# Optimization experiments

Hardware: AMD Instinct MI355X
Metric: run time of the kernel (lower is better)

## Reference

```python
import jax, jax.numpy as jnp
import numpy as np

B, T, D = 8, 1024, 1024
H = 16
DH = D // H  # 64


def setup_inputs() -> dict:
    key = jax.random.key(0)
    k1, k2, k3 = jax.random.split(key, 3)
    x = jax.random.normal(k1, (B, T, D), dtype=jnp.float32)
    W_qkv = jax.random.normal(k2, (3 * D, D), dtype=jnp.float32) * (D ** -0.5)
    W_proj = jax.random.normal(k3, (D, D), dtype=jnp.float32) * (D ** -0.5)
    return {"x": x, "W_qkv": W_qkv, "W_proj": W_proj}


def reference(x, W_qkv, W_proj):
    b, t, _ = x.shape
    # qkv: [B,T,3*D] -> [B,T,3,H,DH]
    qkv = (x @ W_qkv.T).reshape(b, t, 3, H, DH)
    q, k, v = qkv[:, :, 0], qkv[:, :, 1], qkv[:, :, 2]  # [B,T,H,DH]
    scale = DH ** -0.5
    # scores: [B,H,Tq,Tk]
    scores = jnp.einsum("bqhd,bkhd->bhqk", q, k) * scale
    # NOTE: softmax over dim=-2 (the QUERY axis), as in the original module
    attn = jax.nn.softmax(scores, axis=-2)
    out = jnp.einsum("bhqk,bkhd->bqhd", attn, v).reshape(b, t, D)
    return out @ W_proj.T
```

## Files before the change

### kernel.cpp

```cpp
#include <hip/hip_runtime.h>


typedef __bf16 bf16_t;
typedef __bf16 bf16x8 __attribute__((ext_vector_type(8)));
typedef __bf16 bf16x4 __attribute__((ext_vector_type(4)));
typedef float f32x4 __attribute__((ext_vector_type(4)));
typedef unsigned short u16x8 __attribute__((ext_vector_type(8)));

#define DEV __device__ __forceinline__
#define C2 0.18033688f

DEV void gld_lds16(const bf16_t* g, bf16_t* l) {
  __builtin_amdgcn_global_load_lds(
      (const __attribute__((address_space(1))) unsigned int*)g,
      (__attribute__((address_space(3))) unsigned int*)l, 16, 0, 0);
}

DEV float exp2c(float x) { return __builtin_amdgcn_exp2f(fminf(x, 30.f)); }
DEV float sanit(float v) { return (v == v) ? fminf(fmaxf(v, -1e4f), 1e4f) : 0.f; }

DEV int sw64(int r, int kc) { return r * 64 + (((kc ^ (r + (r >> 3))) & 7) << 3); }

DEV f32x4 mfma16(bf16x8 a, bf16x8 b, f32x4 c) {
  return __builtin_amdgcn_mfma_f32_16x16x32_bf16(a, b, c, 0, 0, 0);
}

__global__ void convert_in(const void* __restrict__ x, const void* __restrict__ wq,
                           const void* __restrict__ wp, bf16_t* __restrict__ xb,
                           bf16_t* __restrict__ wqb, bf16_t* __restrict__ wpb,
                           int* __restrict__ flagp) {
  __shared__ int smax;
  if (threadIdx.x == 0) smax = 0;
  __syncthreads();
  {
    int e = (((const unsigned short*)x)[threadIdx.x] >> 7) & 0xFF;
    atomicMax(&smax, e);
  }
  __syncthreads();
  const bool isF32 = smax >= 160;

  int i = blockIdx.x * 256 + threadIdx.x;
  if (i == 0) *flagp = isF32 ? 1 : 0;
  const void* src;
  bf16_t* dst;
  int off;
  bool isQ = false;
  if (i < 1048576) { src = x; dst = xb; off = i; }
  else if (i < 1441792) {
    src = wq; dst = wqb; off = i - 1048576;
    isQ = off < 131072;
  } else { src = wp; dst = wpb; off = i - 1441792; }
  if (isF32) {
    const float s = isQ ? C2 : 1.0f;
    const float4* sp = (const float4*)src;
    float4 a = sp[off * 2], b = sp[off * 2 + 1];
    bf16x8 o;
    o[0] = (bf16_t)(a.x * s); o[1] = (bf16_t)(a.y * s);
    o[2] = (bf16_t)(a.z * s); o[3] = (bf16_t)(a.w * s);
    o[4] = (bf16_t)(b.x * s); o[5] = (bf16_t)(b.y * s);
    o[6] = (bf16_t)(b.z * s); o[7] = (bf16_t)(b.w * s);
    *(bf16x8*)(dst + (size_t)off * 8) = o;
  } else {
    u16x8 v = ((const u16x8*)src)[off];
    if (isQ) {
      bf16x8 bsrc = __builtin_bit_cast(bf16x8, v);
      bf16x8 o;
#pragma unroll
      for (int t = 0; t < 8; ++t) o[t] = (bf16_t)((float)bsrc[t] * C2);
      *(bf16x8*)(dst + (size_t)off * 8) = o;
    } else {
      ((u16x8*)dst)[off] = v;
    }
  }
}

__global__ __launch_bounds__(256, 2)
void gemm_bt(const bf16_t* __restrict__ A, int lda, const bf16_t* __restrict__ B,
             bf16_t* __restrict__ Cb, float* __restrict__ Cf, int ldc,
             int K, const int* __restrict__ f32flag) {
  __shared__ bf16_t sA0[128 * 64];
  __shared__ bf16_t sB0[128 * 64];
  __shared__ bf16_t sA1[128 * 64];
  __shared__ bf16_t sB1[128 * 64];
  const int tid = threadIdx.x;
  const int wave = tid >> 6, lane = tid & 63;
  const int l = lane & 15, quad = lane >> 4;
  const int nwg = gridDim.x * gridDim.y;
  const int bid = blockIdx.y * gridDim.x + blockIdx.x;
  const int sb = (bid & 7) * (nwg >> 3) + (bid >> 3);
  const int row0 = (sb / gridDim.x) * 128, col0 = (sb % gridDim.x) * 128;
  const int wm = (wave >> 1) * 64, wn = (wave & 1) * 64;
  f32x4 acc[4][4];
#pragma unroll
  for (int i = 0; i < 4; ++i)
#pragma unroll
    for (int j = 0; j < 4; ++j) acc[i][j] = f32x4{0.f, 0.f, 0.f, 0.f};

#define STAGE_G(sa, sb_, kk)                                                  \
  {                                                                           \
    _Pragma("unroll") for (int t = 0; t < 4; ++t) {                           \
      int n = t * 256 + tid;                                                  \
      int r = n >> 3;                                                         \
      int kc = ((n & 7) ^ (r + (r >> 3))) & 7;                                \
      gld_lds16(A + (size_t)(row0 + r) * lda + (kk) + kc * 8, (sa) + n * 8);  \
      gld_lds16(B + (size_t)(col0 + r) * K + (kk) + kc * 8, (sb_) + n * 8);   \
    }                                                                         \
  }

#define COMPUTE_G(sa, sb_)                                                    \
  {                                                                           \
    _Pragma("unroll") for (int ks = 0; ks < 2; ++ks) {                        \
      bf16x8 af[4], bfr[4];                                                   \
      _Pragma("unroll") for (int i = 0; i < 4; ++i) af[i] =                   \
          *(const bf16x8*)&(sa)[sw64(wm + i * 16 + l, ks * 4 + quad)];        \
      _Pragma("unroll") for (int j = 0; j < 4; ++j) bfr[j] =                  \
          *(const bf16x8*)&(sb_)[sw64(wn + j * 16 + l, ks * 4 + quad)];       \
      _Pragma("unroll") for (int i = 0; i < 4; ++i)                           \
          _Pragma("unroll") for (int j = 0; j < 4; ++j) acc[i][j] =           \
              mfma16(af[i], bfr[j], acc[i][j]);                               \
    }                                                                         \
  }

  STAGE_G(sA0, sB0, 0);
  for (int k0 = 0; k0 < K; k0 += 128) {
    __syncthreads();
    if (k0 + 64 < K) STAGE_G(sA1, sB1, k0 + 64);
    COMPUTE_G(sA0, sB0);
    __syncthreads();
    if (k0 + 128 < K) STAGE_G(sA0, sB0, k0 + 128);
    COMPUTE_G(sA1, sB1);
  }
#undef STAGE_G
#undef COMPUTE_G

  const bool of32 = (f32flag != nullptr) && (*f32flag != 0);
#pragma unroll
  for (int i = 0; i < 4; ++i) {
    int rr = row0 + wm + i * 16 + quad * 4;
#pragma unroll
    for (int j = 0; j < 4; ++j) {
      int cc = col0 + wn + j * 16 + l;
#pragma unroll
      for (int t = 0; t < 4; ++t) {
        float v = sanit(acc[i][j][t]);
        size_t idx = (size_t)(rr + t) * ldc + cc;
        if (of32) Cf[idx] = v; else Cb[idx] = (bf16_t)v;
      }
    }
  }
}

__global__ __launch_bounds__(256, 4)
void attn_stats(const bf16_t* __restrict__ qkv, bf16_t* __restrict__ Vts) {
  __shared__ bf16_t sK[128 * 64];
  __shared__ bf16_t sV[128 * 64];
  __shared__ float sL[128];
  const int bh = blockIdx.x, kt = blockIdx.y;
  const int b = bh >> 4, h = bh & 15;
  const int tid = threadIdx.x, wave = tid >> 6, lane = tid & 63;
  const int l = lane & 15, quad = lane >> 4;
  const size_t rowK = (size_t)b * 1024 + kt * 128;

#pragma unroll
  for (int t = 0; t < 4; ++t) {
    int base = wave * 256 + t * 64;
    int n = base + lane;
    int r = n >> 3;
    int kc = ((n & 7) ^ (r + (r >> 3))) & 7;
    gld_lds16(qkv + (rowK + r) * 3072 + 2048 + h * 64 + kc * 8, sV + base * 8);
    gld_lds16(qkv + (rowK + r) * 3072 + 1024 + h * 64 + kc * 8, sK + base * 8);
  }
  if (tid < 128) sL[tid] = 0.f;
  __syncthreads();

  float accj[8];
#pragma unroll
  for (int j = 0; j < 8; ++j) accj[j] = 0.f;

  for (int qt = 0; qt < 8; ++qt) {
    bf16x8 aq[2][2];
#pragma unroll
    for (int i = 0; i < 2; ++i)
#pragma unroll
      for (int ks = 0; ks < 2; ++ks)
        aq[i][ks] = *(const bf16x8*)&qkv[((size_t)b * 1024 + qt * 128 + wave * 32 +
                                          i * 16 + l) * 3072 + h * 64 +
                                         (ks * 4 + quad) * 8];
#pragma unroll
    for (int j = 0; j < 8; ++j) {
      f32x4 s0 = {0.f, 0.f, 0.f, 0.f}, s1 = {0.f, 0.f, 0.f, 0.f};
      __builtin_amdgcn_s_setprio(1);
#pragma unroll
      for (int ks = 0; ks < 2; ++ks) {
        bf16x8 bk = *(const bf16x8*)&sK[sw64(j * 16 + l, ks * 4 + quad)];
        s0 = mfma16(aq[0][ks], bk, s0);
        s1 = mfma16(aq[1][ks], bk, s1);
      }
      __builtin_amdgcn_s_setprio(0);
#pragma unroll
      for (int t = 0; t < 4; ++t)
        accj[j] += exp2c(s0[t]) + exp2c(s1[t]);
    }
  }
#pragma unroll
  for (int j = 0; j < 8; ++j) {
    float v = accj[j];
    v += __shfl_xor(v, 16);
    v += __shfl_xor(v, 32);
    if (lane < 16) atomicAdd(&sL[j * 16 + l], v);
  }
  __syncthreads();
  if (tid < 128) sL[tid] = 1.0f / fmaxf(sL[tid], 1e-20f);
  __syncthreads();

#pragma unroll
  for (int t = 0; t < 4; ++t) {
    int u = t * 256 + tid;
    int d = u >> 4, k0 = (u & 15) * 8;
    bf16x8 pk;
#pragma unroll
    for (int i = 0; i < 8; ++i) {
      int kl = (k0 & ~31) | ((i >> 2) << 4) | (((k0 >> 3) & 3) << 2) | (i & 3);
      float v = (float)sV[sw64(kl, d >> 3) + (d & 7)];
      pk[i] = (bf16_t)(v * sL[kl]);
    }
    *(bf16x8*)&Vts[((size_t)bh * 64 + d) * 1024 + kt * 128 + k0] = pk;
  }
}

__global__ __launch_bounds__(512, 4)
void attn_out_k(const bf16_t* __restrict__ qkv, const bf16_t* __restrict__ Vts,
                bf16_t* __restrict__ attn) {
  __shared__ bf16_t sK[2][128 * 64];
  __shared__ bf16_t sV[2][64 * 128];
  const int bh = blockIdx.x, qt = blockIdx.y;
  const int b = bh >> 4, h = bh & 15;
  const int tid = threadIdx.x, wave = tid >> 6, lane = tid & 63;
  const int l = lane & 15, quad = lane >> 4;
  const bf16_t* qbase = qkv + (size_t)b * 3145728 + h * 64;
  const bf16_t* vbase = Vts + (size_t)bh * 65536;

  bf16x8 bq[2][2];
#pragma unroll
  for (int i = 0; i < 2; ++i)
#pragma unroll
    for (int ks = 0; ks < 2; ++ks)
      bq[i][ks] = *(const bf16x8*)&qbase[(size_t)(qt * 256 + wave * 32 + i * 16 + l) *
                                             3072 + ks * 32 + quad * 8];
  f32x4 o[2][4];
#pragma unroll
  for (int i = 0; i < 2; ++i)
#pragma unroll
    for (int jd = 0; jd < 4; ++jd) o[i][jd] = f32x4{0.f, 0.f, 0.f, 0.f};

#pragma unroll
  for (int t = 0; t < 2; ++t) {
    int n = t * 512 + tid;
    int r = n >> 3;
    int kc = ((n & 7) ^ (r + (r >> 3))) & 7;
    gld_lds16(qkv + ((size_t)b * 1024 + r) * 3072 + 1024 + h * 64 + kc * 8,
              sK[0] + n * 8);
    int d = n >> 4, s = n & 15;
    int c = s ^ (d & 7);
    gld_lds16(vbase + (size_t)d * 1024 + c * 8, sV[0] + n * 8);
  }

  for (int kt = 0; kt < 8; ++kt) {
    const int buf = kt & 1;
    __syncthreads();
    if (kt < 7) {
#pragma unroll
      for (int t = 0; t < 2; ++t) {
        int n = t * 512 + tid;
        int r = n >> 3;
        int kc = ((n & 7) ^ (r + (r >> 3))) & 7;
        gld_lds16(qkv + ((size_t)b * 1024 + (kt + 1) * 128 + r) * 3072 + 1024 +
                      h * 64 + kc * 8,
                  sK[buf ^ 1] + n * 8);
        int d = n >> 4, s = n & 15;
        int c = s ^ (d & 7);
        gld_lds16(vbase + (size_t)d * 1024 + (kt + 1) * 128 + c * 8,
                  sV[buf ^ 1] + n * 8);
      }
    }
    const bf16_t* sKb = sK[buf];
    const bf16_t* sVb = sV[buf];

#pragma unroll
    for (int ch = 0; ch < 4; ++ch) {
      bf16x8 ak[2][2];
#pragma unroll
      for (int kk = 0; kk < 2; ++kk)
#pragma unroll
        for (int ks = 0; ks < 2; ++ks)
          ak[kk][ks] = *(const bf16x8*)&sKb[sw64(ch * 32 + kk * 16 + l,
                                                 ks * 4 + quad)];
      bf16x8 va[4];
#pragma unroll
      for (int jd = 0; jd < 4; ++jd)
        va[jd] = *(const bf16x8*)&sVb[(jd * 16 + l) * 128 +
                                      (((ch * 4 + quad) ^ (l & 7)) << 3)];
#pragma unroll
      for (int i = 0; i < 2; ++i) {
        __builtin_amdgcn_s_setprio(1);
        f32x4 st0 = {0.f, 0.f, 0.f, 0.f}, st1 = {0.f, 0.f, 0.f, 0.f};
        st0 = mfma16(ak[0][0], bq[i][0], st0);
        st0 = mfma16(ak[0][1], bq[i][1], st0);
        st1 = mfma16(ak[1][0], bq[i][0], st1);
        st1 = mfma16(ak[1][1], bq[i][1], st1);
        bf16x8 pc;
#pragma unroll
        for (int t = 0; t < 4; ++t) {
          pc[t] = (bf16_t)exp2c(st0[t]);
          pc[4 + t] = (bf16_t)exp2c(st1[t]);
        }
#pragma unroll
        for (int jd = 0; jd < 4; ++jd)
          o[i][jd] = mfma16(va[jd], pc, o[i][jd]);
        __builtin_amdgcn_s_setprio(0);
      }
    }
  }
#pragma unroll
  for (int i = 0; i < 2; ++i) {
    size_t row = (size_t)b * 1024 + qt * 256 + wave * 32 + i * 16 + l;
#pragma unroll
    for (int jd = 0; jd < 4; ++jd) {
      bf16x4 pk;
#pragma unroll
      for (int t = 0; t < 4; ++t) pk[t] = (bf16_t)sanit(o[i][jd][t]);
      *(bf16x4*)&attn[row * 3072 + h * 64 + jd * 16 + quad * 4] = pk;
    }
  }
}

extern "C" void kernel_launch(void* const* d_in, const int* in_sizes, int n_in,
                              void* d_out, int out_size, void* d_ws, size_t ws_size,
                              hipStream_t stream) {
  (void)in_sizes; (void)n_in; (void)out_size; (void)ws_size;
  char* w = (char*)d_ws;
  bf16_t* qkv = (bf16_t*)w;
  bf16_t* xb = (bf16_t*)(w + 50331648);
  bf16_t* Vts = xb;
  bf16_t* Wqkvb = (bf16_t*)(w + 67108864);
  bf16_t* Wprojb = (bf16_t*)(w + 73400320);
  int* flag = (int*)(w + 75497472);
  bf16_t* attn = qkv + 2048;

  convert_in<<<6144, 256, 0, stream>>>(d_in[0], d_in[1], d_in[2],
                                       xb, Wqkvb, Wprojb, flag);

  gemm_bt<<<dim3(24, 64), 256, 0, stream>>>(xb, 1024, Wqkvb, qkv, nullptr, 3072,
                                            1024, nullptr);
  attn_stats<<<dim3(128, 8), 256, 0, stream>>>(qkv, Vts);
  attn_out_k<<<dim3(128, 4), 512, 0, stream>>>(qkv, Vts, attn);
  gemm_bt<<<dim3(8, 64), 256, 0, stream>>>(attn, 3072, Wprojb, (bf16_t*)d_out,
                                           (float*)d_out, 1024, 1024, flag);
}
```

Measured before the change: 262.9 us.

## Double-buffer Q tiles through LDS in attention stats kernel

The column-statistics kernel now stages each 128-row Q tile into LDS with async global-to-LDS loads, double-buffered so the next tile's load overlaps the current tile's MFMA and exp work. Before, Q fragments were read straight from global memory into registers. The V tile is loaded into the freed Q buffer only after the last Q tile is consumed, which keeps LDS use at three tiles. Occupancy is lowered from 4 to 3 blocks per CU, and extra barriers are added per tile pair. The macros are also rewritten as do-while(0) blocks with no speed effect.

```diff
diff --git a/kernel.cpp b/kernel.cpp
--- a/kernel.cpp
+++ b/kernel.cpp
@@ -97,7 +97,7 @@
     for (int j = 0; j < 4; ++j) acc[i][j] = f32x4{0.f, 0.f, 0.f, 0.f};
 
 #define STAGE_G(sa, sb_, kk)                                                  \
-  {                                                                           \
+  do {                                                                        \
     _Pragma("unroll") for (int t = 0; t < 4; ++t) {                           \
       int n = t * 256 + tid;                                                  \
       int r = n >> 3;                                                         \
@@ -105,10 +105,10 @@
       gld_lds16(A + (size_t)(row0 + r) * lda + (kk) + kc * 8, (sa) + n * 8);  \
       gld_lds16(B + (size_t)(col0 + r) * K + (kk) + kc * 8, (sb_) + n * 8);   \
     }                                                                         \
-  }
+  } while (0)
 
 #define COMPUTE_G(sa, sb_)                                                    \
-  {                                                                           \
+  do {                                                                        \
     _Pragma("unroll") for (int ks = 0; ks < 2; ++ks) {                        \
       bf16x8 af[4], bfr[4];                                                   \
       _Pragma("unroll") for (int i = 0; i < 4; ++i) af[i] =                   \
@@ -119,7 +119,7 @@
           _Pragma("unroll") for (int j = 0; j < 4; ++j) acc[i][j] =           \
               mfma16(af[i], bfr[j], acc[i][j]);                               \
     }                                                                         \
-  }
+  } while (0)
 
   STAGE_G(sA0, sB0, 0);
   for (int k0 = 0; k0 < K; k0 += 128) {
@@ -150,10 +150,11 @@
   }
 }
 
-__global__ __launch_bounds__(256, 4)
+__global__ __launch_bounds__(256, 3)
 void attn_stats(const bf16_t* __restrict__ qkv, bf16_t* __restrict__ Vts) {
-  __shared__ bf16_t sK[128 * 64];
-  __shared__ bf16_t sV[128 * 64];
+  __shared__ bf16_t sKp[128 * 64];
+  __shared__ bf16_t sQ0[128 * 64];
+  __shared__ bf16_t sQ1[128 * 64];
   __shared__ float sL[128];
   const int bh = blockIdx.x, kt = blockIdx.y;
   const int b = bh >> 4, h = bh & 15;
@@ -161,14 +162,61 @@
   const int l = lane & 15, quad = lane >> 4;
   const size_t rowK = (size_t)b * 1024 + kt * 128;
 
+#define STAGEQ(dst, qt)                                                       \
+  do {                                                                        \
+    _Pragma("unroll") for (int t = 0; t < 4; ++t) {                           \
+      int base = wave * 256 + t * 64;                                         \
+      int n = base + lane;                                                    \
+      int r = n >> 3;                                                         \
+      int kc = ((n & 7) ^ (r + (r >> 3))) & 7;                                \
+      gld_lds16(qkv + ((size_t)b * 1024 + (qt) * 128 + r) * 3072 + h * 64 +   \
+                    kc * 8,                                                   \
+                (dst) + base * 8);                                            \
+    }                                                                         \
+  } while (0)
+
+#define STAGEV(dst)                                                           \
+  do {                                                                        \
+    _Pragma("unroll") for (int t = 0; t < 4; ++t) {                           \
+      int base = wave * 256 + t * 64;                                         \
+      int n = base + lane;                                                    \
+      int r = n >> 3;                                                         \
+      int kc = ((n & 7) ^ (r + (r >> 3))) & 7;                                \
+      gld_lds16(qkv + (rowK + r) * 3072 + 2048 + h * 64 + kc * 8,             \
+                (dst) + base * 8);                                            \
+    }                                                                         \
+  } while (0)
+
+#define QT_BODY(sQb)                                                          \
+  do {                                                                        \
+    bf16x8 aq[2][2];                                                          \
+    _Pragma("unroll") for (int i2 = 0; i2 < 2; ++i2)                          \
+        _Pragma("unroll") for (int ks = 0; ks < 2; ++ks) aq[i2][ks] =         \
+            *(const bf16x8*)&(sQb)[sw64(wave * 32 + i2 * 16 + l,              \
+                                        ks * 4 + quad)];                      \
+    _Pragma("unroll") for (int j = 0; j < 8; ++j) {                           \
+      f32x4 s0 = {0.f, 0.f, 0.f, 0.f}, s1 = {0.f, 0.f, 0.f, 0.f};            \
+      __builtin_amdgcn_s_setprio(1);                                          \
+      _Pragma("unroll") for (int ks = 0; ks < 2; ++ks) {                      \
+        bf16x8 bk = *(const bf16x8*)&sKp[sw64(j * 16 + l, ks * 4 + quad)];    \
+        s0 = mfma16(aq[0][ks], bk, s0);                                       \
+        s1 = mfma16(aq[1][ks], bk, s1);                                       \
+      }                                                                       \
+      __builtin_amdgcn_s_setprio(0);                                          \
+      _Pragma("unroll") for (int t = 0; t < 4; ++t)                           \
+          accj[j] += exp2c(s0[t]) + exp2c(s1[t]);                             \
+    }                                                                         \
+  } while (0)
+
 #pragma unroll
   for (int t = 0; t < 4; ++t) {
     int base = wave * 256 + t * 64;
     int n = base + lane;
     int r = n >> 3;
     int kc = ((n & 7) ^ (r + (r >> 3))) & 7;
-    gld_lds16(qkv + (rowK + r) * 3072 + 2048 + h * 64 + kc * 8, sV + base * 8);
-    gld_lds16(qkv + (rowK + r) * 3072 + 1024 + h * 64 + kc * 8, sK + base * 8);
+    gld_lds16(qkv + (rowK + r) * 3072 + 1024 + h * 64 + kc * 8, sKp + base * 8);
+    gld_lds16(qkv + ((size_t)b * 1024 + r) * 3072 + h * 64 + kc * 8,
+              sQ0 + base * 8);
   }
   if (tid < 128) sL[tid] = 0.f;
   __syncthreads();
@@ -177,31 +225,23 @@
 #pragma unroll
   for (int j = 0; j < 8; ++j) accj[j] = 0.f;
 
-  for (int qt = 0; qt < 8; ++qt) {
-    bf16x8 aq[2][2];
-#pragma unroll
-    for (int i = 0; i < 2; ++i)
-#pragma unroll
-      for (int ks = 0; ks < 2; ++ks)
-        aq[i][ks] = *(const bf16x8*)&qkv[((size_t)b * 1024 + qt * 128 + wave * 32 +
-                                          i * 16 + l) * 3072 + h * 64 +
-                                         (ks * 4 + quad) * 8];
-#pragma unroll
-    for (int j = 0; j < 8; ++j) {
-      f32x4 s0 = {0.f, 0.f, 0.f, 0.f}, s1 = {0.f, 0.f, 0.f, 0.f};
-      __builtin_amdgcn_s_setprio(1);
-#pragma unroll
-      for (int ks = 0; ks < 2; ++ks) {
-        bf16x8 bk = *(const bf16x8*)&sK[sw64(j * 16 + l, ks * 4 + quad)];
-        s0 = mfma16(aq[0][ks], bk, s0);
-        s1 = mfma16(aq[1][ks], bk, s1);
-      }
-      __builtin_amdgcn_s_setprio(0);
-#pragma unroll
-      for (int t = 0; t < 4; ++t)
-        accj[j] += exp2c(s0[t]) + exp2c(s1[t]);
-    }
-  }
+#pragma unroll
+  for (int qt = 0; qt < 8; qt += 2) {
+    STAGEQ(sQ1, qt + 1);
+    QT_BODY(sQ0);
+    __syncthreads();
+    if (qt + 2 < 8) {
+      STAGEQ(sQ0, qt + 2);
+    } else {
+      STAGEV(sQ0);
+    }
+    QT_BODY(sQ1);
+    __syncthreads();
+  }
+#undef STAGEQ
+#undef STAGEV
+#undef QT_BODY
+
 #pragma unroll
   for (int j = 0; j < 8; ++j) {
     float v = accj[j];
@@ -221,7 +261,7 @@
 #pragma unroll
     for (int i = 0; i < 8; ++i) {
       int kl = (k0 & ~31) | ((i >> 2) << 4) | (((k0 >> 3) & 3) << 2) | (i & 3);
-      float v = (float)sV[sw64(kl, d >> 3) + (d & 7)];
+      float v = (float)sQ0[sw64(kl, d >> 3) + (d & 7)];
       pk[i] = (bf16_t)(v * sL[kl]);
     }
     *(bf16x8*)&Vts[((size_t)bh * 64 + d) * 1024 + kt * 128 + k0] = pk;
```

Result: slower. 621.4 us (+136.4%).
